# Kernel optimization log

Hardware: AMD Instinct MI355X
Metric: run time of the kernel (lower is better)

The kernel has to match this reference:

```python
import jax, jax.numpy as jnp
import numpy as np

B, F, Q = 8192, 128, 64
H1, H2 = 256, 256
THRESHOLD = 0.95
EPS = 1e-12


def setup_inputs() -> dict:
    key = jax.random.key(0)
    ks = jax.random.split(key, 8)
    in_dim = F + 1 + Q  # raw + quantum + graph feature
    def lin(k, fan_in, fan_out):
        bound = 1.0 / np.sqrt(fan_in)
        kw, kb = jax.random.split(k)
        W = jax.random.uniform(kw, (fan_out, fan_in), jnp.float32, -bound, bound)
        b = jax.random.uniform(kb, (fan_out,), jnp.float32, -bound, bound)
        return W, b
    W1, b1 = lin(ks[2], in_dim, H1)
    W2, b2 = lin(ks[3], H1, H2)
    W3, b3 = lin(ks[4], H2, 1)
    return {
        'x': jax.random.normal(ks[0], (B, F), jnp.float32),
        'quantum_features': jax.random.normal(ks[1], (B, Q), jnp.float32),
        'W1': W1, 'b1': b1, 'W2': W2, 'b2': b2, 'W3': W3, 'b3': b3,
    }


def _graph_feat(x):
    # normalized Gram matrix -> squared cosine fidelity -> threshold -> row mean
    xn = x / (jnp.linalg.norm(x, axis=1, keepdims=True) + EPS)  # [B, F]
    fid = jnp.square(xn @ xn.T)                                  # [B, B]
    adj = jnp.where(fid >= THRESHOLD, 1.0, 0.0)
    adj = adj * (1.0 - jnp.eye(x.shape[0], dtype=x.dtype))       # no self-edges
    return jnp.mean(adj, axis=1, keepdims=True)                  # [B, 1]


def reference(x, quantum_features, W1, b1, W2, b2, W3, b3):
    graph_feat = jax.lax.stop_gradient(_graph_feat(x))  # built under no_grad in torch
    feats = jnp.concatenate([x, quantum_features, graph_feat], axis=1)  # [B, F+Q+1]
    h = jax.nn.relu(feats @ W1.T + b1)
    h = jax.nn.relu(h @ W2.T + b2)
    out = h @ W3.T + b3  # [B, 1]
    return out[:, 0]
```

## Files before the change

kernel.cpp:

```cpp
#include <hip/hip_runtime.h>
#include <hip/hip_bf16.h>

typedef __attribute__((ext_vector_type(8))) short bf16x8;
typedef __attribute__((ext_vector_type(8))) int i32x8;
typedef __attribute__((ext_vector_type(4))) float f32x4;
typedef unsigned int uint;
typedef unsigned short u16;

#define NROWS 8192
#define F_DIM 128
#define Q_DIM 64
#define K1    192
#define H_DIM 256
#define APITCH 200

static __device__ inline unsigned short bf_bits(__hip_bfloat16 b) {
  unsigned short u; __builtin_memcpy(&u, &b, 2); return u;
}
static __device__ inline uint packhl(float v) {
  __hip_bfloat16 h = __float2bfloat16(v);
  float hf = __bfloat162float(h);
  __hip_bfloat16 l = __float2bfloat16(v - hf);
  return ((uint)bf_bits(l) << 16) | (uint)bf_bits(h);
}
static __device__ inline void split_hl(float v, unsigned short& h, unsigned short& l) {
  __hip_bfloat16 hb = __float2bfloat16(v);
  float hf = __bfloat162float(hb);
  __hip_bfloat16 lb = __float2bfloat16(v - hf);
  h = bf_bits(hb); l = bf_bits(lb);
}

union uu { uint4 u; bf16x8 v; };

__global__ __launch_bounds__(256) void norm_prep_kernel(const float* __restrict__ x,
                                                        const float* __restrict__ W1,
                                                        const float* __restrict__ W2,
                                                        unsigned char* __restrict__ xn8,
                                                        u16* __restrict__ W1h, u16* __restrict__ W1l,
                                                        u16* __restrict__ W2h, u16* __restrict__ W2l,
                                                        float* __restrict__ W1g,
                                                        int* __restrict__ cnt) {
  int tid = threadIdx.x;
  int bid = blockIdx.x;
  if (bid < 256) {
    u16 h, l; split_hl(W2[bid * 256 + tid], h, l);
    W2h[bid * 256 + tid] = h;
    W2l[bid * 256 + tid] = l;
  } else if (bid < 512) {
    int n = bid - 256;
    if (tid < K1) {
      u16 h, l; split_hl(W1[n * 193 + tid], h, l);
      W1h[n * K1 + tid] = h;
      W1l[n * K1 + tid] = l;
    } else if (tid == K1) {
      W1g[n] = W1[n * 193 + 192];
    }
  }
  if (bid < 32) cnt[bid * 256 + tid] = 0;

  int lane = tid & 63;
  int row = bid * 4 + (tid >> 6);
  const float2 v = *(const float2*)(x + (size_t)row * F_DIM + lane * 2);
  float s = v.x * v.x + v.y * v.y;
#pragma unroll
  for (int off = 32; off; off >>= 1) s += __shfl_xor(s, off);
  float inv = 1.0f / (sqrtf(s) + 1e-12f);
  int pk = __builtin_amdgcn_cvt_pk_fp8_f32(v.x * inv, v.y * inv, 0, 0);
  *(unsigned short*)(xn8 + (size_t)row * F_DIM + lane * 2) = (unsigned short)(pk & 0xffff);
}

__global__ __launch_bounds__(256) void gram8_kernel(const unsigned char* __restrict__ xn8,
                                                    int* __restrict__ cnt) {
  __shared__ char smem[32768];
  int tid = threadIdx.x;
  int lane = tid & 63;
  int wave = tid >> 6;
  int lr = lane & 15;
  int quad = lane >> 4;

  int t = blockIdx.x;
  int bi = (int)((129.0f - sqrtf(129.0f * 129.0f - 8.0f * (float)t)) * 0.5f);
  while ((bi + 1) * (129 - (bi + 1)) / 2 <= t) bi++;
  while (bi * (129 - bi) / 2 > t) bi--;
  int bj = bi + (t - bi * (129 - bi) / 2);
  int i0 = bi * 128, j0 = bj * 128;

#pragma unroll
  for (int it = 0; it < 8; ++it) {
    int half = it >> 2;
    int row = (it & 3) * 32 + (tid >> 3);
    int chunk = tid & 7;
    int grow = (half ? j0 : i0) + row;
    uint4 v = *(const uint4*)(xn8 + (size_t)grow * F_DIM + chunk * 16);
    *(uint4*)(smem + half * 16384 + row * 128 + ((chunk ^ (row & 7)) << 4)) = v;
  }
  __syncthreads();

  int wi = (wave >> 1) * 64, wj = (wave & 1) * 64;

  f32x4 acc[4][4];
#pragma unroll
  for (int i = 0; i < 4; i++)
#pragma unroll
    for (int j = 0; j < 4; j++) acc[i][j] = (f32x4){0.f, 0.f, 0.f, 0.f};

  i32x8 a[4], b[4];
#pragma unroll
  for (int tt = 0; tt < 4; tt++) {
    int r = wi + tt * 16 + lr;
    const char* base = smem + r * 128;
    uint4 lo = *(const uint4*)(base + (((2 * quad) ^ (r & 7)) << 4));
    uint4 hi = *(const uint4*)(base + (((2 * quad + 1) ^ (r & 7)) << 4));
    i32x8 f;
    f[0] = lo.x; f[1] = lo.y; f[2] = lo.z; f[3] = lo.w;
    f[4] = hi.x; f[5] = hi.y; f[6] = hi.z; f[7] = hi.w;
    a[tt] = f;
  }
#pragma unroll
  for (int tt = 0; tt < 4; tt++) {
    int r = wj + tt * 16 + lr;
    const char* base = smem + 16384 + r * 128;
    uint4 lo = *(const uint4*)(base + (((2 * quad) ^ (r & 7)) << 4));
    uint4 hi = *(const uint4*)(base + (((2 * quad + 1) ^ (r & 7)) << 4));
    i32x8 f;
    f[0] = lo.x; f[1] = lo.y; f[2] = lo.z; f[3] = lo.w;
    f[4] = hi.x; f[5] = hi.y; f[6] = hi.z; f[7] = hi.w;
    b[tt] = f;
  }

#pragma unroll
  for (int tr = 0; tr < 4; tr++)
#pragma unroll
    for (int tc = 0; tc < 4; tc++)
      acc[tr][tc] = __builtin_amdgcn_mfma_scale_f32_16x16x128_f8f6f4(
          a[tr], b[tc], acc[tr][tc], 0, 0, 0, 0x7f7f7f7f, 0, 0x7f7f7f7f);

  int i_base = i0 + wi, j_base = j0 + wj;
  bool diag_wave = (i_base == j_base);
  bool offdiag_block = (bi != bj);

  float mx = 0.f;
#pragma unroll
  for (int tr = 0; tr < 4; tr++)
#pragma unroll
    for (int tc = 0; tc < 4; tc++)
#pragma unroll
      for (int r = 0; r < 4; r++) {
        float v = acc[tr][tc][r];
        if (diag_wave && tr == tc && lr == quad * 4 + r) v = 0.f;
        mx = fmaxf(mx, fabsf(v));
      }
  if (__any(mx >= 0.9746f)) {
    for (int tr = 0; tr < 4; tr++)
      for (int tc = 0; tc < 4; tc++)
        for (int r = 0; r < 4; r++) {
          float v = acc[tr][tc][r];
          int row = i_base + tr * 16 + quad * 4 + r;
          int col = j_base + tc * 16 + lr;
          if (v * v >= 0.95f && row != col) {
            atomicAdd(&cnt[row], 1);
            if (offdiag_block) atomicAdd(&cnt[col], 1);
          }
        }
  }
}

__global__ __launch_bounds__(256) void fused_mlp_kernel(const float* __restrict__ x,
                                                        const float* __restrict__ q,
                                                        const u16* __restrict__ W1h,
                                                        const u16* __restrict__ W1l,
                                                        const u16* __restrict__ W2h,
                                                        const u16* __restrict__ W2l,
                                                        const float* __restrict__ W1g,
                                                        const float* __restrict__ b1,
                                                        const float* __restrict__ b2,
                                                        const float* __restrict__ W3,
                                                        const float* __restrict__ b3,
                                                        const int* __restrict__ cnt,
                                                        float* __restrict__ out) {
  __shared__ __align__(16) char smem[58368];
  short* Ahs = (short*)smem;
  short* Als = (short*)(smem + 12800);
  uint*  H1  = (uint*)(smem + 25600);
  float* part = (float*)smem;

  int tid = threadIdx.x;
  int lane = tid & 63;
  int wv = tid >> 6;
  int lr = lane & 15;
  int quad = lane >> 4;
  int mb = blockIdx.x * 32;

  {
    int r = tid >> 3;
    int c8 = (tid & 7) * 4;
#pragma unroll
    for (int it = 0; it < 6; ++it) {
      int col = it * 32 + c8;
      float4 v;
      if (it < 4) v = *(const float4*)(x + (size_t)(mb + r) * F_DIM + col);
      else        v = *(const float4*)(q + (size_t)(mb + r) * Q_DIM + (col - 128));
      unsigned short h0, l0, h1, l1, h2, l2, h3, l3;
      split_hl(v.x, h0, l0); split_hl(v.y, h1, l1);
      split_hl(v.z, h2, l2); split_hl(v.w, h3, l3);
      *(uint2*)&Ahs[r * APITCH + col] = (uint2){(uint)h0 | ((uint)h1 << 16), (uint)h2 | ((uint)h3 << 16)};
      *(uint2*)&Als[r * APITCH + col] = (uint2){(uint)l0 | ((uint)l1 << 16), (uint)l2 | ((uint)l3 << 16)};
    }
  }
  __syncthreads();

  f32x4 acc[2][4];
#pragma unroll
  for (int i = 0; i < 2; i++)
#pragma unroll
    for (int j = 0; j < 4; j++) acc[i][j] = (f32x4){0.f, 0.f, 0.f, 0.f};

  for (int kc = 0; kc < 6; ++kc) {
    int k0 = kc * 32;
    bf16x8 ah[2], al[2], bh[4], bl[4];
#pragma unroll
    for (int tt = 0; tt < 2; ++tt) {
      int row = tt * 16 + lr;
      ah[tt] = *(const bf16x8*)&Ahs[row * APITCH + k0 + quad * 8];
      al[tt] = *(const bf16x8*)&Als[row * APITCH + k0 + quad * 8];
    }
#pragma unroll
    for (int tc = 0; tc < 4; ++tc) {
      int n = wv * 64 + tc * 16 + lr;
      bh[tc] = *(const bf16x8*)(W1h + (size_t)n * K1 + k0 + quad * 8);
      bl[tc] = *(const bf16x8*)(W1l + (size_t)n * K1 + k0 + quad * 8);
    }
#pragma unroll
    for (int tt = 0; tt < 2; ++tt)
#pragma unroll
      for (int tc = 0; tc < 4; ++tc) {
        acc[tt][tc] = __builtin_amdgcn_mfma_f32_16x16x32_bf16(ah[tt], bh[tc], acc[tt][tc], 0, 0, 0);
        acc[tt][tc] = __builtin_amdgcn_mfma_f32_16x16x32_bf16(ah[tt], bl[tc], acc[tt][tc], 0, 0, 0);
        acc[tt][tc] = __builtin_amdgcn_mfma_f32_16x16x32_bf16(al[tt], bh[tc], acc[tt][tc], 0, 0, 0);
      }
  }

  {
    float gv[2][4];
#pragma unroll
    for (int tt = 0; tt < 2; ++tt)
#pragma unroll
      for (int r = 0; r < 4; ++r)
        gv[tt][r] = (float)cnt[mb + tt * 16 + quad * 4 + r] * (1.0f / 8192.0f);
#pragma unroll
    for (int tc = 0; tc < 4; ++tc) {
      int n = wv * 64 + tc * 16 + lr;
      float w = W1g[n];
#pragma unroll
      for (int tt = 0; tt < 2; ++tt)
#pragma unroll
        for (int r = 0; r < 4; ++r)
          acc[tt][tc][r] += gv[tt][r] * w;
    }
  }

#pragma unroll
  for (int tc = 0; tc < 4; ++tc) {
    int n = wv * 64 + tc * 16 + lr;
    float bv = b1[n];
    int g = n >> 2, jj = n & 3;
#pragma unroll
    for (int tt = 0; tt < 2; ++tt)
#pragma unroll
      for (int r = 0; r < 4; ++r) {
        int row = tt * 16 + quad * 4 + r;
        float v = fmaxf(acc[tt][tc][r] + bv, 0.f);
        H1[row * 256 + ((g ^ (row & 31)) * 4 + jj)] = packhl(v);
      }
  }
#pragma unroll
  for (int i = 0; i < 2; i++)
#pragma unroll
    for (int j = 0; j < 4; j++) acc[i][j] = (f32x4){0.f, 0.f, 0.f, 0.f};
  __syncthreads();

  for (int kc = 0; kc < 8; ++kc) {
    bf16x8 ah[2], al[2], bh[4], bl[4];
#pragma unroll
    for (int tt = 0; tt < 2; ++tt) {
      int row = tt * 16 + lr;
      int cb = kc * 8 + quad * 2;
      uint4 u0 = *(const uint4*)&H1[row * 256 + ((cb ^ (row & 31)) * 4)];
      uint4 u1 = *(const uint4*)&H1[row * 256 + (((cb + 1) ^ (row & 31)) * 4)];
      uu h, l;
      h.u.x = (u0.x & 0xffffu) | (u0.y << 16);
      h.u.y = (u0.z & 0xffffu) | (u0.w << 16);
      h.u.z = (u1.x & 0xffffu) | (u1.y << 16);
      h.u.w = (u1.z & 0xffffu) | (u1.w << 16);
      l.u.x = (u0.x >> 16) | (u0.y & 0xffff0000u);
      l.u.y = (u0.z >> 16) | (u0.w & 0xffff0000u);
      l.u.z = (u1.x >> 16) | (u1.y & 0xffff0000u);
      l.u.w = (u1.z >> 16) | (u1.w & 0xffff0000u);
      ah[tt] = h.v; al[tt] = l.v;
    }
#pragma unroll
    for (int tc = 0; tc < 4; ++tc) {
      int n = wv * 64 + tc * 16 + lr;
      bh[tc] = *(const bf16x8*)(W2h + (size_t)n * 256 + kc * 32 + quad * 8);
      bl[tc] = *(const bf16x8*)(W2l + (size_t)n * 256 + kc * 32 + quad * 8);
    }
#pragma unroll
    for (int tt = 0; tt < 2; ++tt)
#pragma unroll
      for (int tc = 0; tc < 4; ++tc) {
        acc[tt][tc] = __builtin_amdgcn_mfma_f32_16x16x32_bf16(ah[tt], bh[tc], acc[tt][tc], 0, 0, 0);
        acc[tt][tc] = __builtin_amdgcn_mfma_f32_16x16x32_bf16(ah[tt], bl[tc], acc[tt][tc], 0, 0, 0);
        acc[tt][tc] = __builtin_amdgcn_mfma_f32_16x16x32_bf16(al[tt], bh[tc], acc[tt][tc], 0, 0, 0);
      }
  }

  float s[2][4];
#pragma unroll
  for (int tt = 0; tt < 2; ++tt)
#pragma unroll
    for (int r = 0; r < 4; ++r) s[tt][r] = 0.f;
#pragma unroll
  for (int tc = 0; tc < 4; ++tc) {
    int n = wv * 64 + tc * 16 + lr;
    float bv = b2[n];
    float w3 = W3[n];
#pragma unroll
    for (int tt = 0; tt < 2; ++tt)
#pragma unroll
      for (int r = 0; r < 4; ++r)
        s[tt][r] += fmaxf(acc[tt][tc][r] + bv, 0.f) * w3;
  }
#pragma unroll
  for (int tt = 0; tt < 2; ++tt)
#pragma unroll
    for (int r = 0; r < 4; ++r) {
      s[tt][r] += __shfl_xor(s[tt][r], 1);
      s[tt][r] += __shfl_xor(s[tt][r], 2);
      s[tt][r] += __shfl_xor(s[tt][r], 4);
      s[tt][r] += __shfl_xor(s[tt][r], 8);
    }
  if (lr == 0) {
#pragma unroll
    for (int tt = 0; tt < 2; ++tt)
#pragma unroll
      for (int r = 0; r < 4; ++r)
        part[wv * 32 + tt * 16 + quad * 4 + r] = s[tt][r];
  }
  __syncthreads();
  if (tid < 32)
    out[mb + tid] = part[tid] + part[32 + tid] + part[64 + tid] + part[96 + tid] + b3[0];
}

extern "C" void kernel_launch(void* const* d_in, const int* in_sizes, int n_in,
                              void* d_out, int out_size, void* d_ws, size_t ws_size,
                              hipStream_t stream) {
  const float* x  = (const float*)d_in[0];
  const float* q  = (const float*)d_in[1];
  const float* W1 = (const float*)d_in[2];
  const float* b1 = (const float*)d_in[3];
  const float* W2 = (const float*)d_in[4];
  const float* b2 = (const float*)d_in[5];
  const float* W3 = (const float*)d_in[6];
  const float* b3 = (const float*)d_in[7];
  float* out = (float*)d_out;

  char* ws = (char*)d_ws;
  unsigned char* xn8 = (unsigned char*)(ws);
  int*   cnt = (int*)(ws + 0x100000);
  u16*   W1h = (u16*)(ws + 0x110000);
  u16*   W1l = (u16*)(ws + 0x128000);
  u16*   W2h = (u16*)(ws + 0x140000);
  u16*   W2l = (u16*)(ws + 0x160000);
  float* W1g = (float*)(ws + 0x180000);

  norm_prep_kernel<<<dim3(2048), dim3(256), 0, stream>>>(x, W1, W2, xn8, W1h, W1l, W2h, W2l, W1g, cnt);
  gram8_kernel<<<dim3(2080), dim3(256), 0, stream>>>(xn8, cnt);
  fused_mlp_kernel<<<dim3(256), dim3(256), 0, stream>>>(x, q, W1h, W1l, W2h, W2l, W1g, b1, b2, W3, b3, cnt, out);
}
```

Baseline: 95.23 us.

## Move weight split into gram kernel and prefetch MLP weight fragments

Result: no change. 94.20 us (-1.1%).

```diff
diff --git a/kernel.cpp b/kernel.cpp
--- a/kernel.cpp
+++ b/kernel.cpp
@@ -33,29 +33,10 @@
 union uu { uint4 u; bf16x8 v; };
 
 __global__ __launch_bounds__(256) void norm_prep_kernel(const float* __restrict__ x,
-                                                        const float* __restrict__ W1,
-                                                        const float* __restrict__ W2,
                                                         unsigned char* __restrict__ xn8,
-                                                        u16* __restrict__ W1h, u16* __restrict__ W1l,
-                                                        u16* __restrict__ W2h, u16* __restrict__ W2l,
-                                                        float* __restrict__ W1g,
                                                         int* __restrict__ cnt) {
   int tid = threadIdx.x;
   int bid = blockIdx.x;
-  if (bid < 256) {
-    u16 h, l; split_hl(W2[bid * 256 + tid], h, l);
-    W2h[bid * 256 + tid] = h;
-    W2l[bid * 256 + tid] = l;
-  } else if (bid < 512) {
-    int n = bid - 256;
-    if (tid < K1) {
-      u16 h, l; split_hl(W1[n * 193 + tid], h, l);
-      W1h[n * K1 + tid] = h;
-      W1l[n * K1 + tid] = l;
-    } else if (tid == K1) {
-      W1g[n] = W1[n * 193 + 192];
-    }
-  }
   if (bid < 32) cnt[bid * 256 + tid] = 0;
 
   int lane = tid & 63;
@@ -70,15 +51,39 @@
 }
 
 __global__ __launch_bounds__(256) void gram8_kernel(const unsigned char* __restrict__ xn8,
-                                                    int* __restrict__ cnt) {
+                                                    int* __restrict__ cnt,
+                                                    const float* __restrict__ W1,
+                                                    const float* __restrict__ W2,
+                                                    u16* __restrict__ W1h, u16* __restrict__ W1l,
+                                                    u16* __restrict__ W2h, u16* __restrict__ W2l,
+                                                    float* __restrict__ W1g) {
+  int tid = threadIdx.x;
+  int t = blockIdx.x;
+  if (t >= 2080) {
+    int b = t - 2080;
+    if (b < 256) {
+      u16 h, l; split_hl(W2[b * 256 + tid], h, l);
+      W2h[b * 256 + tid] = h;
+      W2l[b * 256 + tid] = l;
+    } else {
+      int n = b - 256;
+      if (tid < K1) {
+        u16 h, l; split_hl(W1[n * 193 + tid], h, l);
+        W1h[n * K1 + tid] = h;
+        W1l[n * K1 + tid] = l;
+      } else if (tid == K1) {
+        W1g[n] = W1[n * 193 + 192];
+      }
+    }
+    return;
+  }
+
   __shared__ char smem[32768];
-  int tid = threadIdx.x;
   int lane = tid & 63;
   int wave = tid >> 6;
   int lr = lane & 15;
   int quad = lane >> 4;
 
-  int t = blockIdx.x;
   int bi = (int)((129.0f - sqrtf(129.0f * 129.0f - 8.0f * (float)t)) * 0.5f);
   while ((bi + 1) * (129 - (bi + 1)) / 2 <= t) bi++;
   while (bi * (129 - bi) / 2 > t) bi--;
@@ -191,6 +196,30 @@
   int quad = lane >> 4;
   int mb = blockIdx.x * 32;
 
+  float bv1[4], bv2[4], w3v[4], w1gv[4];
+#pragma unroll
+  for (int tc = 0; tc < 4; ++tc) {
+    int n = wv * 64 + tc * 16 + lr;
+    bv1[tc] = b1[n];
+    bv2[tc] = b2[n];
+    w3v[tc] = W3[n];
+    w1gv[tc] = W1g[n];
+  }
+  float gv[2][4];
+#pragma unroll
+  for (int tt = 0; tt < 2; ++tt)
+#pragma unroll
+    for (int r = 0; r < 4; ++r)
+      gv[tt][r] = (float)cnt[mb + tt * 16 + quad * 4 + r] * (1.0f / 8192.0f);
+
+  size_t base1 = (size_t)(wv * 64 + lr) * K1 + quad * 8;
+  bf16x8 pw1h[4], pw1l[4];
+#pragma unroll
+  for (int tc = 0; tc < 4; ++tc) {
+    pw1h[tc] = *(const bf16x8*)(W1h + base1 + (size_t)tc * 16 * K1);
+    pw1l[tc] = *(const bf16x8*)(W1l + base1 + (size_t)tc * 16 * K1);
+  }
+
   {
     int r = tid >> 3;
     int c8 = (tid & 7) * 4;
@@ -215,9 +244,18 @@
 #pragma unroll
     for (int j = 0; j < 4; j++) acc[i][j] = (f32x4){0.f, 0.f, 0.f, 0.f};
 
+#pragma unroll
   for (int kc = 0; kc < 6; ++kc) {
     int k0 = kc * 32;
-    bf16x8 ah[2], al[2], bh[4], bl[4];
+    bf16x8 nw1h[4], nw1l[4];
+    if (kc < 5) {
+#pragma unroll
+      for (int tc = 0; tc < 4; ++tc) {
+        nw1h[tc] = *(const bf16x8*)(W1h + base1 + (size_t)tc * 16 * K1 + (kc + 1) * 32);
+        nw1l[tc] = *(const bf16x8*)(W1l + base1 + (size_t)tc * 16 * K1 + (kc + 1) * 32);
+      }
+    }
+    bf16x8 ah[2], al[2];
 #pragma unroll
     for (int tt = 0; tt < 2; ++tt) {
       int row = tt * 16 + lr;
@@ -225,44 +263,41 @@
       al[tt] = *(const bf16x8*)&Als[row * APITCH + k0 + quad * 8];
     }
 #pragma unroll
-    for (int tc = 0; tc < 4; ++tc) {
-      int n = wv * 64 + tc * 16 + lr;
-      bh[tc] = *(const bf16x8*)(W1h + (size_t)n * K1 + k0 + quad * 8);
-      bl[tc] = *(const bf16x8*)(W1l + (size_t)n * K1 + k0 + quad * 8);
-    }
-#pragma unroll
     for (int tt = 0; tt < 2; ++tt)
 #pragma unroll
       for (int tc = 0; tc < 4; ++tc) {
-        acc[tt][tc] = __builtin_amdgcn_mfma_f32_16x16x32_bf16(ah[tt], bh[tc], acc[tt][tc], 0, 0, 0);
-        acc[tt][tc] = __builtin_amdgcn_mfma_f32_16x16x32_bf16(ah[tt], bl[tc], acc[tt][tc], 0, 0, 0);
-        acc[tt][tc] = __builtin_amdgcn_mfma_f32_16x16x32_bf16(al[tt], bh[tc], acc[tt][tc], 0, 0, 0);
-      }
-  }
-
-  {
-    float gv[2][4];
+        acc[tt][tc] = __builtin_amdgcn_mfma_f32_16x16x32_bf16(ah[tt], pw1h[tc], acc[tt][tc], 0, 0, 0);
+        acc[tt][tc] = __builtin_amdgcn_mfma_f32_16x16x32_bf16(ah[tt], pw1l[tc], acc[tt][tc], 0, 0, 0);
+        acc[tt][tc] = __builtin_amdgcn_mfma_f32_16x16x32_bf16(al[tt], pw1h[tc], acc[tt][tc], 0, 0, 0);
+      }
+    if (kc < 5) {
+#pragma unroll
+      for (int tc = 0; tc < 4; ++tc) { pw1h[tc] = nw1h[tc]; pw1l[tc] = nw1l[tc]; }
+    }
+  }
+
+  size_t base2 = (size_t)(wv * 64 + lr) * 256 + quad * 8;
+  bf16x8 pw2h[4], pw2l[4];
+#pragma unroll
+  for (int tc = 0; tc < 4; ++tc) {
+    pw2h[tc] = *(const bf16x8*)(W2h + base2 + (size_t)tc * 16 * 256);
+    pw2l[tc] = *(const bf16x8*)(W2l + base2 + (size_t)tc * 16 * 256);
+  }
+
+#pragma unroll
+  for (int tc = 0; tc < 4; ++tc) {
+    float w = w1gv[tc];
 #pragma unroll
     for (int tt = 0; tt < 2; ++tt)
 #pragma unroll
       for (int r = 0; r < 4; ++r)
-        gv[tt][r] = (float)cnt[mb + tt * 16 + quad * 4 + r] * (1.0f / 8192.0f);
-#pragma unroll
-    for (int tc = 0; tc < 4; ++tc) {
-      int n = wv * 64 + tc * 16 + lr;
-      float w = W1g[n];
-#pragma unroll
-      for (int tt = 0; tt < 2; ++tt)
-#pragma unroll
-        for (int r = 0; r < 4; ++r)
-          acc[tt][tc][r] += gv[tt][r] * w;
-    }
+        acc[tt][tc][r] += gv[tt][r] * w;
   }
 
 #pragma unroll
   for (int tc = 0; tc < 4; ++tc) {
     int n = wv * 64 + tc * 16 + lr;
-    float bv = b1[n];
+    float bv = bv1[tc];
     int g = n >> 2, jj = n & 3;
 #pragma unroll
     for (int tt = 0; tt < 2; ++tt)
@@ -279,8 +314,17 @@
     for (int j = 0; j < 4; j++) acc[i][j] = (f32x4){0.f, 0.f, 0.f, 0.f};
   __syncthreads();
 
+#pragma unroll
   for (int kc = 0; kc < 8; ++kc) {
-    bf16x8 ah[2], al[2], bh[4], bl[4];
+    bf16x8 nw2h[4], nw2l[4];
+    if (kc < 7) {
+#pragma unroll
+      for (int tc = 0; tc < 4; ++tc) {
+        nw2h[tc] = *(const bf16x8*)(W2h + base2 + (size_t)tc * 16 * 256 + (kc + 1) * 32);
+        nw2l[tc] = *(const bf16x8*)(W2l + base2 + (size_t)tc * 16 * 256 + (kc + 1) * 32);
+      }
+    }
+    bf16x8 ah[2], al[2];
 #pragma unroll
     for (int tt = 0; tt < 2; ++tt) {
       int row = tt * 16 + lr;
@@ -299,19 +343,17 @@
       ah[tt] = h.v; al[tt] = l.v;
     }
 #pragma unroll
-    for (int tc = 0; tc < 4; ++tc) {
-      int n = wv * 64 + tc * 16 + lr;
-      bh[tc] = *(const bf16x8*)(W2h + (size_t)n * 256 + kc * 32 + quad * 8);
-      bl[tc] = *(const bf16x8*)(W2l + (size_t)n * 256 + kc * 32 + quad * 8);
-    }
-#pragma unroll
     for (int tt = 0; tt < 2; ++tt)
 #pragma unroll
       for (int tc = 0; tc < 4; ++tc) {
-        acc[tt][tc] = __builtin_amdgcn_mfma_f32_16x16x32_bf16(ah[tt], bh[tc], acc[tt][tc], 0, 0, 0);
-        acc[tt][tc] = __builtin_amdgcn_mfma_f32_16x16x32_bf16(ah[tt], bl[tc], acc[tt][tc], 0, 0, 0);
-        acc[tt][tc] = __builtin_amdgcn_mfma_f32_16x16x32_bf16(al[tt], bh[tc], acc[tt][tc], 0, 0, 0);
-      }
+        acc[tt][tc] = __builtin_amdgcn_mfma_f32_16x16x32_bf16(ah[tt], pw2h[tc], acc[tt][tc], 0, 0, 0);
+        acc[tt][tc] = __builtin_amdgcn_mfma_f32_16x16x32_bf16(ah[tt], pw2l[tc], acc[tt][tc], 0, 0, 0);
+        acc[tt][tc] = __builtin_amdgcn_mfma_f32_16x16x32_bf16(al[tt], pw2h[tc], acc[tt][tc], 0, 0, 0);
+      }
+    if (kc < 7) {
+#pragma unroll
+      for (int tc = 0; tc < 4; ++tc) { pw2h[tc] = nw2h[tc]; pw2l[tc] = nw2l[tc]; }
+    }
   }
 
   float s[2][4];
@@ -321,9 +363,8 @@
     for (int r = 0; r < 4; ++r) s[tt][r] = 0.f;
 #pragma unroll
   for (int tc = 0; tc < 4; ++tc) {
-    int n = wv * 64 + tc * 16 + lr;
-    float bv = b2[n];
-    float w3 = W3[n];
+    float bv = bv2[tc];
+    float w3 = w3v[tc];
 #pragma unroll
     for (int tt = 0; tt < 2; ++tt)
 #pragma unroll
@@ -373,7 +414,7 @@
   u16*   W2l = (u16*)(ws + 0x160000);
   float* W1g = (float*)(ws + 0x180000);
 
-  norm_prep_kernel<<<dim3(2048), dim3(256), 0, stream>>>(x, W1, W2, xn8, W1h, W1l, W2h, W2l, W1g, cnt);
-  gram8_kernel<<<dim3(2080), dim3(256), 0, stream>>>(xn8, cnt);
+  norm_prep_kernel<<<dim3(2048), dim3(256), 0, stream>>>(x, xn8, cnt);
+  gram8_kernel<<<dim3(2592), dim3(256), 0, stream>>>(xn8, cnt, W1, W2, W1h, W1l, W2h, W2l, W1g);
   fused_mlp_kernel<<<dim3(256), dim3(256), 0, stream>>>(x, q, W1h, W1l, W2h, W2l, W1g, b1, b2, W3, b3, cnt, out);
 }
```
